# Kernel tuning notes

Measured on AMD Instinct MI355X. Metric: run time of the kernel, lower is better.

The kernel has to match this reference:

```python
import jax, jax.numpy as jnp
import numpy as np

RNN_SIZE = 256
FC_DIM = 64
IMG_DIM = 3200
EMB_DIM = 300


def setup_inputs() -> dict:
    key = jax.random.key(0)
    ks = jax.random.split(key, 16)
    n, L = 64, 512
    s = 0.02
    return {
        "img_feats": jax.random.normal(ks[0], (n, L, IMG_DIM), jnp.float32),
        "phrase_emb": jax.random.normal(ks[1], (n, EMB_DIM), jnp.float32),
        "masks": jnp.ones((n, L), jnp.float32),
        "select_ixs": jax.random.randint(ks[2], (n,), 0, L),
        # cnn_fc_layer: Linear(3200 -> 64)
        "W_cnn": jax.random.normal(ks[3], (IMG_DIM, FC_DIM), jnp.float32) * s,
        "b_cnn": jnp.zeros((FC_DIM,), jnp.float32),
        # phrase_embed: Linear(300 -> 64)
        "W_phr": jax.random.normal(ks[4], (EMB_DIM, FC_DIM), jnp.float32) * s,
        "b_phr": jnp.zeros((FC_DIM,), jnp.float32),
        # LSTMCell(64 -> 256), gate order i,f,g,o as in torch
        "W_ih": jax.random.normal(ks[5], (FC_DIM, 4 * RNN_SIZE), jnp.float32) * s,
        "b_ih": jnp.zeros((4 * RNN_SIZE,), jnp.float32),
        "W_hh": jax.random.normal(ks[6], (RNN_SIZE, 4 * RNN_SIZE), jnp.float32) * s,
        "b_hh": jnp.zeros((4 * RNN_SIZE,), jnp.float32),
        # classifier: Linear(256 -> 64) -> ReLU -> Linear(64 -> 2) -> LogSoftmax
        "W_c1": jax.random.normal(ks[7], (RNN_SIZE, FC_DIM), jnp.float32) * s,
        "b_c1": jnp.zeros((FC_DIM,), jnp.float32),
        "W_c2": jax.random.normal(ks[8], (FC_DIM, 2), jnp.float32) * s,
        "b_c2": jnp.zeros((2,), jnp.float32),
    }


def _forward(img_feats, phrase_emb, select_ixs,
             W_cnn, b_cnn, W_phr, b_phr,
             W_ih, b_ih, W_hh, b_hh,
             W_c1, b_c1, W_c2, b_c2):
    n, L, _ = img_feats.shape
    # per-step small FCs, vectorized over time (dropout is inference no-op)
    img_fc = jax.nn.relu(jnp.einsum('nld,df->nlf', img_feats, W_cnn) + b_cnn)  # (n,L,64)
    emb = jax.nn.relu(phrase_emb @ W_phr + b_phr)                               # (n,64)
    fuse = img_fc * emb[:, None, :]                                             # (n,L,64)

    def cell(carry, x_t):
        h, c = carry
        gates = x_t @ W_ih + b_ih + h @ W_hh + b_hh        # (n, 4*H)
        i, f, g, o = jnp.split(gates, 4, axis=-1)
        i, f, o = jax.nn.sigmoid(i), jax.nn.sigmoid(f), jax.nn.sigmoid(o)
        g = jnp.tanh(g)
        c = f * c + i * g
        h = o * jnp.tanh(c)
        return (h, c), h

    h0 = jnp.zeros((n, RNN_SIZE), fuse.dtype)
    c0 = jnp.zeros((n, RNN_SIZE), fuse.dtype)
    _, hs = jax.lax.scan(cell, (h0, c0), jnp.swapaxes(fuse, 0, 1))  # (L,n,H)
    output_feats = jnp.swapaxes(hs, 0, 1)                           # (n,L,H)

    hid = jax.nn.relu(jnp.einsum('nlh,hf->nlf', output_feats, W_c1) + b_c1)
    logits = jnp.einsum('nlf,fk->nlk', hid, W_c2) + b_c2
    logprobs = jax.nn.log_softmax(logits, axis=-1)                  # (n,L,2)

    selected = jnp.take_along_axis(output_feats, select_ixs[:, None, None], axis=1)[:, 0, :]
    return logprobs, output_feats, selected


def reference(img_feats, phrase_emb, masks, select_ixs,
              W_cnn, b_cnn, W_phr, b_phr,
              W_ih, b_ih, W_hh, b_hh,
              W_c1, b_c1, W_c2, b_c2):
    # masks is accepted but unused, as in the original forward()
    return _forward(img_feats, phrase_emb, select_ixs,
                    W_cnn, b_cnn, W_phr, b_phr,
                    W_ih, b_ih, W_hh, b_hh,
                    W_c1, b_c1, W_c2, b_c2)
```

## Files before the change

kernel.cpp:

```cpp
#include <hip/hip_runtime.h>
#include <hip/hip_bf16.h>
#include <stdint.h>

#define LSEQ 512
#define NB   64
#define IMGD 3200
#define EMBD 300
#define HD   256
#define KCH  10

typedef __bf16 bf16x8 __attribute__((ext_vector_type(8)));
typedef float  f32x4  __attribute__((ext_vector_type(4)));

__device__ __forceinline__ unsigned short f2bf(float x) {
  unsigned u = __builtin_bit_cast(unsigned, x);
  u = (u + 0x7FFFu + ((u >> 16) & 1u)) >> 16;
  return (unsigned short)u;
}

__global__ __launch_bounds__(256) void k1_init_emb(
    const float* __restrict__ phr, const float* __restrict__ Wp,
    const float* __restrict__ bp, const float* __restrict__ Wih,
    const float* __restrict__ Whh, float* __restrict__ emb,
    unsigned* __restrict__ hbuf, unsigned short* __restrict__ Wpk) {
  int tid = threadIdx.x, blk = blockIdx.x;
  int gid = blk * 256 + tid;
  if (gid < 16384) {
    hbuf[gid] = 0u;
    hbuf[gid + 16384] = 0u;
  }
  for (int e = gid; e < 327680; e += 16384) {
    int j = e & 7;
    int t1 = e >> 3;
    int l = t1 & 63;
    int t2 = t1 >> 6;
    int kk = t2 % 10;
    int t3 = t2 / 10;
    int g = t3 & 3, w = (t3 >> 2) & 3, j4 = t3 >> 4;
    int k = kk * 32 + ((l >> 4) << 3) + j;
    int col = g * 256 + j4 * 64 + w * 16 + (l & 15);
    float v = (k < 256) ? Whh[k * 1024 + col] : Wih[(k - 256) * 1024 + col];
    Wpk[e] = f2bf(v);
  }
  if (blk < 16) {
    int b = gid >> 6, f = gid & 63;
    float acc = bp[f];
    for (int k = 0; k < EMBD; ++k) acc += phr[b * EMBD + k] * Wp[k * 64 + f];
    emb[gid] = fmaxf(acc, 0.f);
  }
}

__global__ __launch_bounds__(256) void k2_imgfuse(
    const float* __restrict__ img, const float* __restrict__ Wc,
    const float* __restrict__ bc, const float* __restrict__ emb,
    unsigned short* __restrict__ fuse) {
  __shared__ float sX[32 * 65];
  __shared__ float sW[64 * 64];
  int tid = threadIdx.x, blk = blockIdx.x;
  int r = tid & 31, g = tid >> 5;
  int rs = tid >> 3, cs = (tid & 7) * 8;
  float acc[8];
#pragma unroll
  for (int j = 0; j < 8; ++j) acc[j] = 0.f;

  for (int k0 = 0; k0 < IMGD; k0 += 64) {
    const float* xsrc = img + (size_t)(blk * 32 + rs) * IMGD + k0 + cs;
    float4 v0 = *(const float4*)xsrc;
    float4 v1 = *(const float4*)(xsrc + 4);
    float* xd = sX + rs * 65 + cs;
    xd[0]=v0.x; xd[1]=v0.y; xd[2]=v0.z; xd[3]=v0.w;
    xd[4]=v1.x; xd[5]=v1.y; xd[6]=v1.z; xd[7]=v1.w;
    const float4* wsrc = (const float4*)(Wc + k0 * 64);
#pragma unroll
    for (int i = 0; i < 4; ++i) ((float4*)sW)[i * 256 + tid] = wsrc[i * 256 + tid];
    __syncthreads();
#pragma unroll 8
    for (int k = 0; k < 64; ++k) {
      float xv = sX[r * 65 + k];
      const float* wr = sW + k * 64 + g * 8;
      float4 wa = *(const float4*)wr;
      float4 wb = *(const float4*)(wr + 4);
      acc[0] += xv * wa.x; acc[1] += xv * wa.y; acc[2] += xv * wa.z; acc[3] += xv * wa.w;
      acc[4] += xv * wb.x; acc[5] += xv * wb.y; acc[6] += xv * wb.z; acc[7] += xv * wb.w;
    }
    __syncthreads();
  }
  int rowg = blk * 32 + r;
  int b = rowg >> 9;
  unsigned pk[4];
#pragma unroll
  for (int j2 = 0; j2 < 4; ++j2) {
    int c = g * 8 + j2 * 2;
    float v0 = fmaxf(acc[j2 * 2] + bc[c], 0.f) * emb[b * 64 + c];
    float v1 = fmaxf(acc[j2 * 2 + 1] + bc[c + 1], 0.f) * emb[b * 64 + c + 1];
    pk[j2] = (unsigned)f2bf(v0) | ((unsigned)f2bf(v1) << 16);
  }
  *(uint4*)(fuse + (size_t)rowg * 64 + g * 8) = make_uint4(pk[0], pk[1], pk[2], pk[3]);
}

__global__ __launch_bounds__(256) void k3_lstm(
    const unsigned short* __restrict__ Wpk,
    const float* __restrict__ bih, const float* __restrict__ bhh,
    const unsigned short* __restrict__ fuse,
    unsigned* __restrict__ hbuf, float* __restrict__ outfeats) {
  __shared__ __align__(16) unsigned short sZ[2][16 * 328];
  int tid = threadIdx.x;
  int wg  = blockIdx.x;
  int grp = wg & 3;
  int j4  = wg >> 2;
  int b0  = grp * 16;
  int w = tid >> 6, l = tid & 63;
  int q = l >> 4, c = l & 15;

  bf16x8 Bf[4][KCH];
  const bf16x8* wp = (const bf16x8*)Wpk + (size_t)((j4 * 4 + w) * 4) * KCH * 64 + l;
#pragma unroll
  for (int g = 0; g < 4; ++g)
#pragma unroll
    for (int kk = 0; kk < KCH; ++kk)
      Bf[g][kk] = wp[(g * KCH + kk) * 64];
  float bv[4];
#pragma unroll
  for (int g = 0; g < 4; ++g) {
    int colg = g * 256 + j4 * 64 + w * 16 + c;
    bv[g] = bih[colg] + bhh[colg];
  }

  int row = tid >> 4, u16i = tid & 15;
  const unsigned short* fbase = fuse + ((size_t)(b0 + row) * 512) * 64 + u16i * 4;
  unsigned short* zh[2] = {&sZ[0][row * 328 + u16i * 16], &sZ[1][row * 328 + u16i * 16]};
  unsigned short* zx[2] = {&sZ[0][row * 328 + 256 + u16i * 4], &sZ[1][row * 328 + 256 + u16i * 4]};
  const unsigned short* za[2] = {&sZ[0][c * 328 + q * 8], &sZ[1][c * 328 + q * 8]};

  int u = j4 * 64 + w * 16 + c;
  float cst[4] = {0.f, 0.f, 0.f, 0.f};
  float* ob = outfeats + ((size_t)(b0 + q * 4) * 512) * 256 + u;
  unsigned* mb = hbuf + (size_t)(b0 + q * 4) * 256 + u;

  for (int step = 0; step < LSEQ; ++step) {
    int p = step & 1;
    uint2 fv = *(const uint2*)(fbase + (size_t)step * 64);
    const unsigned long long* pb =
        (const unsigned long long*)(hbuf + p * 16384 + (b0 + row) * 256 + u16i * 16);
    unsigned long long want = (unsigned long long)(step & 0xFFFF);
    unsigned long long m[8];
    for (;;) {
      bool ok = true;
#pragma unroll
      for (int i = 0; i < 8; ++i)
        m[i] = __hip_atomic_load(pb + i, __ATOMIC_RELAXED, __HIP_MEMORY_SCOPE_SYSTEM);
#pragma unroll
      for (int i = 0; i < 8; ++i)
        ok = ok && (((m[i] >> 16) & 0xFFFFull) == want) && ((m[i] >> 48) == want);
      if (ok) break;
    }
    unsigned o0 = (unsigned)((m[0] & 0xFFFFull) | ((m[0] >> 16) & 0xFFFF0000ull));
    unsigned o1 = (unsigned)((m[1] & 0xFFFFull) | ((m[1] >> 16) & 0xFFFF0000ull));
    unsigned o2 = (unsigned)((m[2] & 0xFFFFull) | ((m[2] >> 16) & 0xFFFF0000ull));
    unsigned o3 = (unsigned)((m[3] & 0xFFFFull) | ((m[3] >> 16) & 0xFFFF0000ull));
    unsigned o4 = (unsigned)((m[4] & 0xFFFFull) | ((m[4] >> 16) & 0xFFFF0000ull));
    unsigned o5 = (unsigned)((m[5] & 0xFFFFull) | ((m[5] >> 16) & 0xFFFF0000ull));
    unsigned o6 = (unsigned)((m[6] & 0xFFFFull) | ((m[6] >> 16) & 0xFFFF0000ull));
    unsigned o7 = (unsigned)((m[7] & 0xFFFFull) | ((m[7] >> 16) & 0xFFFF0000ull));
    unsigned short* zhp = p ? zh[1] : zh[0];
    ((uint4*)zhp)[0] = make_uint4(o0, o1, o2, o3);
    ((uint4*)zhp)[1] = make_uint4(o4, o5, o6, o7);
    *(uint2*)(p ? zx[1] : zx[0]) = fv;
    __syncthreads();
    const unsigned short* zap = p ? za[1] : za[0];
    f32x4 a0 = {bv[0], bv[0], bv[0], bv[0]};
    f32x4 a1 = {bv[1], bv[1], bv[1], bv[1]};
    f32x4 a2 = {bv[2], bv[2], bv[2], bv[2]};
    f32x4 a3 = {bv[3], bv[3], bv[3], bv[3]};
#pragma unroll
    for (int kk = 0; kk < KCH; ++kk) {
      bf16x8 A = *(const bf16x8*)(zap + kk * 32);
      a0 = __builtin_amdgcn_mfma_f32_16x16x32_bf16(A, Bf[0][kk], a0, 0, 0, 0);
      a1 = __builtin_amdgcn_mfma_f32_16x16x32_bf16(A, Bf[1][kk], a1, 0, 0, 0);
      a2 = __builtin_amdgcn_mfma_f32_16x16x32_bf16(A, Bf[2][kk], a2, 0, 0, 0);
      a3 = __builtin_amdgcn_mfma_f32_16x16x32_bf16(A, Bf[3][kk], a3, 0, 0, 0);
    }
    unsigned tag = (unsigned)((step + 1) & 0xFFFF) << 16;
    unsigned* mbp = mb + ((~step & 1) << 14);
#pragma unroll
    for (int r = 0; r < 4; ++r) {
      float zi = a0[r], zf = a1[r], zg = a2[r], zo = a3[r];
      float si = 1.f / (1.f + __expf(-zi));
      float sf = 1.f / (1.f + __expf(-zf));
      float so = 1.f / (1.f + __expf(-zo));
      float e2g = __expf(2.f * zg);
      float tg = (e2g - 1.f) / (e2g + 1.f);
      cst[r] = sf * cst[r] + si * tg;
      float e2c = __expf(2.f * cst[r]);
      float hn = so * (e2c - 1.f) / (e2c + 1.f);
      __hip_atomic_store(mbp + r * 256, tag | (unsigned)f2bf(hn),
                         __ATOMIC_RELAXED, __HIP_MEMORY_SCOPE_SYSTEM);
      ob[((size_t)r * 512 + step) * 256] = hn;
    }
  }
}

__global__ __launch_bounds__(256) void k4_classifier(
    const float* __restrict__ feats, const float* __restrict__ Wc1,
    const float* __restrict__ bc1, const float* __restrict__ Wc2,
    const float* __restrict__ bc2, float* __restrict__ lp) {
  __shared__ float sW[64 * 64];
  __shared__ float sX[16 * 257];
  __shared__ float sH[16 * 68];
  int tid = threadIdx.x, blk = blockIdx.x;
  {
    int rs = tid >> 4, seg = (tid & 15) * 16;
    const float4* src = (const float4*)(feats + (size_t)(blk * 16 + rs) * 256 + seg);
    float* xd = sX + rs * 257 + seg;
#pragma unroll
    for (int i = 0; i < 4; ++i) {
      float4 v = src[i];
      xd[i*4+0]=v.x; xd[i*4+1]=v.y; xd[i*4+2]=v.z; xd[i*4+3]=v.w;
    }
  }
  int r = tid & 15, g = tid >> 4;
  float acc[4] = {0.f, 0.f, 0.f, 0.f};
  for (int c4 = 0; c4 < 4; ++c4) {
    __syncthreads();
#pragma unroll
    for (int i = 0; i < 4; ++i)
      ((float4*)sW)[i * 256 + tid] = ((const float4*)(Wc1 + c4 * 4096))[i * 256 + tid];
    __syncthreads();
#pragma unroll 8
    for (int k = 0; k < 64; ++k) {
      float xv = sX[r * 257 + c4 * 64 + k];
      float4 wv = *(const float4*)(sW + k * 64 + g * 4);
      acc[0] += xv * wv.x; acc[1] += xv * wv.y; acc[2] += xv * wv.z; acc[3] += xv * wv.w;
    }
  }
#pragma unroll
  for (int j = 0; j < 4; ++j) {
    int c = g * 4 + j;
    sH[r * 68 + c] = fmaxf(acc[j] + bc1[c], 0.f);
  }
  __syncthreads();
  if (tid < 16) {
    float l0 = bc2[0], l1 = bc2[1];
    for (int c = 0; c < 64; ++c) {
      float h = sH[tid * 68 + c];
      l0 += h * Wc2[c * 2]; l1 += h * Wc2[c * 2 + 1];
    }
    float mx = fmaxf(l0, l1);
    float lse = mx + logf(__expf(l0 - mx) + __expf(l1 - mx));
    int rowg = blk * 16 + tid;
    lp[rowg * 2]     = l0 - lse;
    lp[rowg * 2 + 1] = l1 - lse;
  }
}

__global__ __launch_bounds__(256) void k5_select(
    const float* __restrict__ feats, const int* __restrict__ six,
    float* __restrict__ sel) {
  int b = blockIdx.x, tid = threadIdx.x;
  int ix = six[b];
  sel[b * 256 + tid] = feats[((size_t)b * 512 + ix) * 256 + tid];
}

extern "C" void kernel_launch(void* const* d_in, const int* in_sizes, int n_in,
                              void* d_out, int out_size, void* d_ws, size_t ws_size,
                              hipStream_t stream) {
  const float* img = (const float*)d_in[0];
  const float* phr = (const float*)d_in[1];
  const int*   six = (const int*)d_in[3];
  const float* Wc  = (const float*)d_in[4];
  const float* bc  = (const float*)d_in[5];
  const float* Wp  = (const float*)d_in[6];
  const float* bp  = (const float*)d_in[7];
  const float* Wih = (const float*)d_in[8];
  const float* bih = (const float*)d_in[9];
  const float* Whh = (const float*)d_in[10];
  const float* bhh = (const float*)d_in[11];
  const float* Wc1 = (const float*)d_in[12];
  const float* bc1 = (const float*)d_in[13];
  const float* Wc2 = (const float*)d_in[14];
  const float* bc2 = (const float*)d_in[15];

  float* out_lp   = (float*)d_out;
  float* out_feat = out_lp + 65536;
  float* out_sel  = out_feat + 8388608;

  char* ws = (char*)d_ws;
  float*          emb   = (float*)ws;
  unsigned short* fuse  = (unsigned short*)(ws + 16384);
  unsigned*       hbuf  = (unsigned*)(ws + 4210688);
  unsigned short* Wpk   = (unsigned short*)(ws + 4341760);

  hipLaunchKernelGGL(k1_init_emb, dim3(64), dim3(256), 0, stream,
                     phr, Wp, bp, Wih, Whh, emb, hbuf, Wpk);
  hipLaunchKernelGGL(k2_imgfuse, dim3(1024), dim3(256), 0, stream,
                     img, Wc, bc, emb, fuse);
  hipLaunchKernelGGL(k3_lstm, dim3(16), dim3(256), 0, stream,
                     Wpk, bih, bhh, fuse, hbuf, out_feat);
  hipLaunchKernelGGL(k4_classifier, dim3(2048), dim3(256), 0, stream,
                     out_feat, Wc1, bc1, Wc2, bc2, out_lp);
  hipLaunchKernelGGL(k5_select, dim3(64), dim3(256), 0, stream,
                     out_feat, six, out_sel);
}
```

Measured before the change: 2.127 ms.

## Split LSTM batch across 32 workgroups and use agent-scope atomics

The recurrent LSTM kernel now splits the batch into 8 groups of 8 rows instead of 4 groups of 16, doubling the workgroup count so more CUs handle the serial time loop. Each block polls less hidden state per step, and only half the MFMA output rows (q<2) are used, so half the 16-row MFMA tile is wasted. Spin loads and stores on the hidden-state buffer drop from system scope to agent scope to cut cross-workgroup synchronisation latency. The cost is more blocks taking part in the per-step global handshake.

```diff
diff --git a/kernel.cpp b/kernel.cpp
--- a/kernel.cpp
+++ b/kernel.cpp
@@ -98,17 +98,17 @@
   *(uint4*)(fuse + (size_t)rowg * 64 + g * 8) = make_uint4(pk[0], pk[1], pk[2], pk[3]);
 }
 
-__global__ __launch_bounds__(256) void k3_lstm(
+__global__ __launch_bounds__(256, 1) void k3_lstm(
     const unsigned short* __restrict__ Wpk,
     const float* __restrict__ bih, const float* __restrict__ bhh,
     const unsigned short* __restrict__ fuse,
     unsigned* __restrict__ hbuf, float* __restrict__ outfeats) {
-  __shared__ __align__(16) unsigned short sZ[2][16 * 328];
+  __shared__ __align__(16) unsigned short sZ[2][8 * 328];
   int tid = threadIdx.x;
   int wg  = blockIdx.x;
-  int grp = wg & 3;
-  int j4  = wg >> 2;
-  int b0  = grp * 16;
+  int grp = wg & 7;
+  int j4  = wg >> 3;
+  int b0  = grp * 8;
   int w = tid >> 6, l = tid & 63;
   int q = l >> 4, c = l & 15;
 
@@ -126,11 +126,11 @@
     bv[g] = bih[colg] + bhh[colg];
   }
 
-  int row = tid >> 4, u16i = tid & 15;
-  const unsigned short* fbase = fuse + ((size_t)(b0 + row) * 512) * 64 + u16i * 4;
-  unsigned short* zh[2] = {&sZ[0][row * 328 + u16i * 16], &sZ[1][row * 328 + u16i * 16]};
-  unsigned short* zx[2] = {&sZ[0][row * 328 + 256 + u16i * 4], &sZ[1][row * 328 + 256 + u16i * 4]};
-  const unsigned short* za[2] = {&sZ[0][c * 328 + q * 8], &sZ[1][c * 328 + q * 8]};
+  int row = tid >> 5, u8i = tid & 31;
+  const unsigned short* fbase = fuse + ((size_t)(b0 + row) * 512) * 64 + u8i * 2;
+  unsigned short* zh[2] = {&sZ[0][row * 328 + u8i * 8], &sZ[1][row * 328 + u8i * 8]};
+  unsigned short* zx[2] = {&sZ[0][row * 328 + 256 + u8i * 2], &sZ[1][row * 328 + 256 + u8i * 2]};
+  const unsigned short* za[2] = {&sZ[0][(c & 7) * 328 + q * 8], &sZ[1][(c & 7) * 328 + q * 8]};
 
   int u = j4 * 64 + w * 16 + c;
   float cst[4] = {0.f, 0.f, 0.f, 0.f};
@@ -139,18 +139,18 @@
 
   for (int step = 0; step < LSEQ; ++step) {
     int p = step & 1;
-    uint2 fv = *(const uint2*)(fbase + (size_t)step * 64);
+    unsigned fv = *(const unsigned*)(fbase + (size_t)step * 64);
     const unsigned long long* pb =
-        (const unsigned long long*)(hbuf + p * 16384 + (b0 + row) * 256 + u16i * 16);
+        (const unsigned long long*)(hbuf + p * 16384 + (b0 + row) * 256 + u8i * 8);
     unsigned long long want = (unsigned long long)(step & 0xFFFF);
-    unsigned long long m[8];
+    unsigned long long m[4];
     for (;;) {
       bool ok = true;
 #pragma unroll
-      for (int i = 0; i < 8; ++i)
-        m[i] = __hip_atomic_load(pb + i, __ATOMIC_RELAXED, __HIP_MEMORY_SCOPE_SYSTEM);
-#pragma unroll
-      for (int i = 0; i < 8; ++i)
+      for (int i = 0; i < 4; ++i)
+        m[i] = __hip_atomic_load(pb + i, __ATOMIC_RELAXED, __HIP_MEMORY_SCOPE_AGENT);
+#pragma unroll
+      for (int i = 0; i < 4; ++i)
         ok = ok && (((m[i] >> 16) & 0xFFFFull) == want) && ((m[i] >> 48) == want);
       if (ok) break;
     }
@@ -158,14 +158,8 @@
     unsigned o1 = (unsigned)((m[1] & 0xFFFFull) | ((m[1] >> 16) & 0xFFFF0000ull));
     unsigned o2 = (unsigned)((m[2] & 0xFFFFull) | ((m[2] >> 16) & 0xFFFF0000ull));
     unsigned o3 = (unsigned)((m[3] & 0xFFFFull) | ((m[3] >> 16) & 0xFFFF0000ull));
-    unsigned o4 = (unsigned)((m[4] & 0xFFFFull) | ((m[4] >> 16) & 0xFFFF0000ull));
-    unsigned o5 = (unsigned)((m[5] & 0xFFFFull) | ((m[5] >> 16) & 0xFFFF0000ull));
-    unsigned o6 = (unsigned)((m[6] & 0xFFFFull) | ((m[6] >> 16) & 0xFFFF0000ull));
-    unsigned o7 = (unsigned)((m[7] & 0xFFFFull) | ((m[7] >> 16) & 0xFFFF0000ull));
-    unsigned short* zhp = p ? zh[1] : zh[0];
-    ((uint4*)zhp)[0] = make_uint4(o0, o1, o2, o3);
-    ((uint4*)zhp)[1] = make_uint4(o4, o5, o6, o7);
-    *(uint2*)(p ? zx[1] : zx[0]) = fv;
+    *(uint4*)(p ? zh[1] : zh[0]) = make_uint4(o0, o1, o2, o3);
+    *(unsigned*)(p ? zx[1] : zx[0]) = fv;
     __syncthreads();
     const unsigned short* zap = p ? za[1] : za[0];
     f32x4 a0 = {bv[0], bv[0], bv[0], bv[0]};
@@ -180,22 +174,24 @@
       a2 = __builtin_amdgcn_mfma_f32_16x16x32_bf16(A, Bf[2][kk], a2, 0, 0, 0);
       a3 = __builtin_amdgcn_mfma_f32_16x16x32_bf16(A, Bf[3][kk], a3, 0, 0, 0);
     }
-    unsigned tag = (unsigned)((step + 1) & 0xFFFF) << 16;
-    unsigned* mbp = mb + ((~step & 1) << 14);
-#pragma unroll
-    for (int r = 0; r < 4; ++r) {
-      float zi = a0[r], zf = a1[r], zg = a2[r], zo = a3[r];
-      float si = 1.f / (1.f + __expf(-zi));
-      float sf = 1.f / (1.f + __expf(-zf));
-      float so = 1.f / (1.f + __expf(-zo));
-      float e2g = __expf(2.f * zg);
-      float tg = (e2g - 1.f) / (e2g + 1.f);
-      cst[r] = sf * cst[r] + si * tg;
-      float e2c = __expf(2.f * cst[r]);
-      float hn = so * (e2c - 1.f) / (e2c + 1.f);
-      __hip_atomic_store(mbp + r * 256, tag | (unsigned)f2bf(hn),
-                         __ATOMIC_RELAXED, __HIP_MEMORY_SCOPE_SYSTEM);
-      ob[((size_t)r * 512 + step) * 256] = hn;
+    if (q < 2) {
+      unsigned tag = (unsigned)((step + 1) & 0xFFFF) << 16;
+      unsigned* mbp = mb + ((~step & 1) << 14);
+#pragma unroll
+      for (int r = 0; r < 4; ++r) {
+        float zi = a0[r], zf = a1[r], zg = a2[r], zo = a3[r];
+        float si = 1.f / (1.f + __expf(-zi));
+        float sf = 1.f / (1.f + __expf(-zf));
+        float so = 1.f / (1.f + __expf(-zo));
+        float e2g = __expf(2.f * zg);
+        float tg = (e2g - 1.f) / (e2g + 1.f);
+        cst[r] = sf * cst[r] + si * tg;
+        float e2c = __expf(2.f * cst[r]);
+        float hn = so * (e2c - 1.f) / (e2c + 1.f);
+        __hip_atomic_store(mbp + r * 256, tag | (unsigned)f2bf(hn),
+                           __ATOMIC_RELAXED, __HIP_MEMORY_SCOPE_AGENT);
+        ob[((size_t)r * 512 + step) * 256] = hn;
+      }
     }
   }
 }
@@ -294,7 +290,7 @@
                      phr, Wp, bp, Wih, Whh, emb, hbuf, Wpk);
   hipLaunchKernelGGL(k2_imgfuse, dim3(1024), dim3(256), 0, stream,
                      img, Wc, bc, emb, fuse);
-  hipLaunchKernelGGL(k3_lstm, dim3(16), dim3(256), 0, stream,
+  hipLaunchKernelGGL(k3_lstm, dim3(32), dim3(256), 0, stream,
                      Wpk, bih, bhh, fuse, hbuf, out_feat);
   hipLaunchKernelGGL(k4_classifier, dim3(2048), dim3(256), 0, stream,
                      out_feat, Wc1, bc1, Wc2, bc2, out_lp);
```

Result: faster. 1.783 ms (-16.2%).
